# Performance work log

Hardware: AMD Instinct MI355X
Metric: run time of the kernel (lower is better)

## Reference

```python
import jax, jax.numpy as jnp
import numpy as np

DIM = 512
H = 8
HD = DIM // H
MAX_DIST = 128
TABLE = (2 * MAX_DIST + 1) ** 2
LAMBDA_INIT = 0.8


def setup_inputs() -> dict:
    key = jax.random.key(0)
    ks = jax.random.split(key, 20)
    B, Nq, Nkv = 4, 1024, 1024
    inp = {
        "x_q": jax.random.normal(ks[0], (B, Nq, DIM), jnp.float32),
        "x_kv": jax.random.normal(ks[1], (B, Nkv, DIM), jnp.float32),
        "coords_q": jax.random.randint(ks[2], (B, Nq, 2), 0, 256, jnp.int32),
        "coords_k": jax.random.randint(ks[3], (B, Nkv, 2), 0, 256, jnp.int32),
        "alpha_map": jax.random.uniform(ks[4], (B, Nq, 1), jnp.float32),
        "Wq": jax.random.normal(ks[5], (DIM, DIM), jnp.float32) * 0.02,
        "bq": jnp.zeros((DIM,), jnp.float32),
        "Wk": jax.random.normal(ks[6], (DIM, DIM), jnp.float32) * 0.02,
        "bk": jnp.zeros((DIM,), jnp.float32),
        "Wv": jax.random.normal(ks[7], (DIM, DIM), jnp.float32) * 0.02,
        "bv": jnp.zeros((DIM,), jnp.float32),
        "lambda_q1": jax.random.normal(ks[8], (H // 2, HD), jnp.float32) * 0.1,
        "lambda_k1": jax.random.normal(ks[9], (H // 2, HD), jnp.float32) * 0.1,
        "lambda_q2": jax.random.normal(ks[10], (H // 2, HD), jnp.float32) * 0.1,
        "lambda_k2": jax.random.normal(ks[11], (H // 2, HD), jnp.float32) * 0.1,
        "rpe_table": jax.random.normal(ks[12], (TABLE, H), jnp.float32) * 0.02,
        "Wp": jax.random.normal(ks[13], (DIM, DIM), jnp.float32) * 0.02,
        "bp": jnp.zeros((DIM,), jnp.float32),
    }
    return inp


def reference(x_q, x_kv, coords_q, coords_k, alpha_map,
              Wq, bq, Wk, bk, Wv, bv,
              lambda_q1, lambda_k1, lambda_q2, lambda_k2,
              rpe_table, Wp, bp):
    B, Nq, C = x_q.shape
    Nkv = x_kv.shape[1]
    n_half = H // 2
    scale = HD ** -0.5

    # projections -> [B, H, N, HD]
    q = (x_q @ Wq.T + bq).reshape(B, Nq, H, HD).transpose(0, 2, 1, 3)
    k = (x_kv @ Wk.T + bk).reshape(B, Nkv, H, HD).transpose(0, 2, 1, 3)
    v = (x_kv @ Wv.T + bv).reshape(B, Nkv, H, HD).transpose(0, 2, 1, 3)

    # sparse relative position bias: gather per-pair from table
    rel = coords_q[:, :, None, :] - coords_k[:, None, :, :] + MAX_DIST  # [B,Nq,Nkv,2]
    rel = jnp.clip(rel, 0, 2 * MAX_DIST)
    idx = rel[..., 0] * (2 * MAX_DIST + 1) + rel[..., 1]  # [B,Nq,Nkv]
    bias = rpe_table[idx].transpose(0, 3, 1, 2)  # [B,H,Nq,Nkv]

    scores = jnp.einsum('bhqd,bhkd->bhqk', q, k) * scale + bias
    probs = jax.nn.softmax(scores, axis=-1)
    x_std = jnp.einsum('bhqk,bhkd->bhqd', probs, v)

    lam1 = jnp.exp(jnp.sum(lambda_q1 * lambda_k1, axis=-1))  # [n_half]
    lam2 = jnp.exp(jnp.sum(lambda_q2 * lambda_k2, axis=-1))
    lam = (lam1 - lam2 + LAMBDA_INIT)[None, :, None, None]

    attn_diff = probs[:, :n_half] - lam * probs[:, n_half:]
    x_diff = jnp.einsum('bhqk,bhkd->bhqd', attn_diff, v[:, :n_half])

    alpha = alpha_map[:, None]  # [B,1,Nq,1]
    x1 = x_std[:, :n_half] + alpha * x_diff
    x = jnp.concatenate([x1, x_std[:, n_half:]], axis=1)  # [B,H,Nq,HD]
    x = x.transpose(0, 2, 1, 3).reshape(B, Nq, C)
    return x @ Wp.T + bp
```

## Files before the change

### kernel.cpp

```cpp
#include <hip/hip_runtime.h>
#include <cstddef>
#include <cstdint>

#define DIM   512
#define NSEQ  1024
#define NB    4
#define LOG2E 1.44269504f

typedef unsigned short u16;
typedef short bf16x8 __attribute__((ext_vector_type(8)));
typedef _Float16 half8v __attribute__((ext_vector_type(8)));
typedef float f32x4  __attribute__((ext_vector_type(4)));

#define MFMA(a, b, c)  __builtin_amdgcn_mfma_f32_16x16x32_bf16(a, b, c, 0, 0, 0)
#define MFMAH(a, b, c) __builtin_amdgcn_mfma_f32_16x16x32_f16(a, b, c, 0, 0, 0)

__device__ inline void split2(float x, u16& h, u16& l) {
  unsigned u = __float_as_uint(x);
  unsigned hb = (u + 0x7fffu + ((u >> 16) & 1u)) >> 16;
  float fh = __uint_as_float(hb << 16);
  float r = x - fh;
  unsigned v = __float_as_uint(r);
  unsigned lb = (v + 0x7fffu + ((v >> 16) & 1u)) >> 16;
  h = (u16)hb; l = (u16)lb;
}

__device__ inline uint2 pack4(const u16 a[4]) {
  return make_uint2((unsigned)a[0] | ((unsigned)a[1] << 16),
                    (unsigned)a[2] | ((unsigned)a[3] << 16));
}

__device__ inline u16 f2h(float x) {
  _Float16 h = (_Float16)x;
  u16 r; __builtin_memcpy(&r, &h, 2);
  return r;
}
__device__ inline float h2f(u16 b) {
  _Float16 h; __builtin_memcpy(&h, &b, 2);
  return (float)h;
}
__device__ inline unsigned pkh2(float a, float b) {
  return (unsigned)f2h(a) | ((unsigned)f2h(b) << 16);
}

__device__ inline void split_body(const float* __restrict__ in,
                                  u16* __restrict__ out, int e4) {
  const int e = e4 * 4;
  const int m = e >> 9, c = e & 511;
  const float4 v = *(const float4*)(in + e);
  u16 h[4], l[4];
  split2(v.x, h[0], l[0]); split2(v.y, h[1], l[1]);
  split2(v.z, h[2], l[2]); split2(v.w, h[3], l[3]);
  u16* o = out + (size_t)m * 1024 + c;
  *(uint2*)o = pack4(h);
  *(uint2*)(o + 512) = pack4(l);
}

#define GLDS(g, l)                                                        \
  __builtin_amdgcn_global_load_lds(                                       \
      (const __attribute__((address_space(1))) void*)(g),                 \
      (__attribute__((address_space(3))) void*)(l), 16, 0, 0)

__global__ __launch_bounds__(256) void prep(
    const float* __restrict__ wq, const float* __restrict__ wk,
    const float* __restrict__ wv, const float* __restrict__ wp,
    const float* __restrict__ xq, const float* __restrict__ xkv,
    const int* __restrict__ cq, const int* __restrict__ ck,
    const float* __restrict__ rpe,
    u16* __restrict__ w2, u16* __restrict__ xq2, u16* __restrict__ xkv2,
    u16* __restrict__ biasT) {
  __shared__ u16 Ts[8 * 16 * 64];
  const int id = blockIdx.x;
  const int t = threadIdx.x;
  if (id < 1024) {
    const int y = id >> 8;
    const float* src = (y == 0) ? wq : (y == 1) ? wk : (y == 2) ? wv : wp;
    split_body(src, w2 + (size_t)y * 524288, (id & 255) * 256 + t);
  } else if (id < 5120) {
    const int e = id - 1024;
    const int y = e >> 11;
    split_body(y ? xkv : xq, y ? xkv2 : xq2, (e & 2047) * 256 + t);
  } else {
    const int e = id - 5120;
    const int q0 = (e & 15) * 64, k0 = ((e >> 4) & 63) * 16, b = e >> 10;
    const int qn = t & 63, kb = t >> 6;
    const int2 cqv = ((const int2*)cq)[b * NSEQ + q0 + qn];
#pragma unroll
    for (int j = 0; j < 4; ++j) {
      const int k = kb * 4 + j;
      const int2 ckv = ((const int2*)ck)[b * NSEQ + k0 + k];
      const int r0 = min(max(cqv.x - ckv.x + 128, 0), 256);
      const int r1 = min(max(cqv.y - ckv.y + 128, 0), 256);
      const float* rp = rpe + (size_t)(r0 * 257 + r1) * 8;
      const float4 f0 = *(const float4*)rp;
      const float4 f1 = *(const float4*)(rp + 4);
      u16* dst = Ts + k * 64 + qn;
      dst[0 * 1024] = f2h(f0.x * LOG2E); dst[1 * 1024] = f2h(f0.y * LOG2E);
      dst[2 * 1024] = f2h(f0.z * LOG2E); dst[3 * 1024] = f2h(f0.w * LOG2E);
      dst[4 * 1024] = f2h(f1.x * LOG2E); dst[5 * 1024] = f2h(f1.y * LOG2E);
      dst[6 * 1024] = f2h(f1.z * LOG2E); dst[7 * 1024] = f2h(f1.w * LOG2E);
    }
    __syncthreads();
#pragma unroll
    for (int i = 0; i < 4; ++i) {
      const int e2 = i * 256 + t;
      const int row = e2 >> 3, c8 = e2 & 7;
      const int hh = row >> 4, k = row & 15;
      const uint4 v = *(const uint4*)(Ts + row * 64 + c8 * 8);
      *(uint4*)(biasT + ((size_t)(b * 8 + hh) * 1024 + k0 + k) * 1024 +
                q0 + c8 * 8) = v;
    }
  }
}

template <int OUT_MODE>
__device__ __forceinline__ void gemm128(
    u16* __restrict__ Ah, u16* __restrict__ Al,
    u16* __restrict__ Bh, u16* __restrict__ Bl,
    const u16* __restrict__ A2, const u16* __restrict__ B2,
    const float* __restrict__ bias, void* __restrict__ outp,
    float scale, int m0, int n0) {
  const int tid = threadIdx.x;
  const int lane = tid & 63, w = tid >> 6;
  const int wm = (w & 1) * 64, wn = (w >> 1) * 32;
  const int lr = lane >> 3;
  const int scc = (lane & 7) ^ lr;

  const u16* gA = A2 + (size_t)(m0 + w * 32 + lr) * 1024 + scc * 8;
  const u16* gB = B2 + (size_t)(n0 + w * 16 + lr) * 1024 + scc * 8;
  char* lAh = (char*)Ah + w * 4096;  char* lAl = (char*)Al + w * 4096;
  char* lBh = (char*)Bh + w * 2048;  char* lBl = (char*)Bl + w * 2048;

  const int fr = lane & 15, kq = lane >> 4, fx = fr & 7;
  int aoff[2][4], boff[2][2];
#pragma unroll
  for (int s = 0; s < 2; ++s) {
#pragma unroll
    for (int i = 0; i < 4; ++i)
      aoff[s][i] = (wm + i * 16 + fr) * 64 + (((s * 4 + kq) ^ fx)) * 8;
#pragma unroll
    for (int j = 0; j < 2; ++j)
      boff[s][j] = (wn + j * 16 + fr) * 64 + (((s * 4 + kq) ^ fx)) * 8;
  }

  f32x4 acc[4][2] = {};
  for (int k0 = 0; k0 < 512; k0 += 64) {
    __syncthreads();
#pragma unroll
    for (int i = 0; i < 4; ++i) {
      GLDS(gA + (size_t)i * 8192 + k0, lAh + i * 1024);
      GLDS(gA + (size_t)i * 8192 + 512 + k0, lAl + i * 1024);
    }
#pragma unroll
    for (int i = 0; i < 2; ++i) {
      GLDS(gB + (size_t)i * 8192 + k0, lBh + i * 1024);
      GLDS(gB + (size_t)i * 8192 + 512 + k0, lBl + i * 1024);
    }
    __syncthreads();
#pragma unroll
    for (int s = 0; s < 2; ++s) {
      bf16x8 ah[4], al[4], bh[2], bl[2];
#pragma unroll
      for (int i = 0; i < 4; ++i) {
        ah[i] = *(const bf16x8*)(Ah + aoff[s][i]);
        al[i] = *(const bf16x8*)(Al + aoff[s][i]);
      }
#pragma unroll
      for (int j = 0; j < 2; ++j) {
        bh[j] = *(const bf16x8*)(Bh + boff[s][j]);
        bl[j] = *(const bf16x8*)(Bl + boff[s][j]);
      }
#pragma unroll
      for (int i = 0; i < 4; ++i)
#pragma unroll
        for (int j = 0; j < 2; ++j) {
          acc[i][j] = MFMA(al[i], bh[j], acc[i][j]);
          acc[i][j] = MFMA(ah[i], bl[j], acc[i][j]);
          acc[i][j] = MFMA(ah[i], bh[j], acc[i][j]);
        }
    }
  }

  const int er = (lane >> 4) * 4, ec = lane & 15;
#pragma unroll
  for (int i = 0; i < 4; ++i)
#pragma unroll
    for (int j = 0; j < 2; ++j) {
      const int row = m0 + wm + i * 16 + er;
      const int col = n0 + wn + j * 16 + ec;
      const float bv = bias[col];
      if (OUT_MODE == 4) {
        u16 hf[4];
#pragma unroll
        for (int r = 0; r < 4; ++r) hf[r] = f2h((acc[i][j][r] + bv) * scale);
        const int bb = row >> 10, kk = row & 1023;
        *(uint2*)((u16*)outp + ((size_t)(bb * 512 + col)) * 1024 + kk) =
            pack4(hf);
      } else {
#pragma unroll
        for (int r = 0; r < 4; ++r) {
          const float v = (acc[i][j][r] + bv) * scale;
          if (OUT_MODE == 3)
            ((u16*)outp)[(size_t)(row + r) * 512 + col] = f2h(v);
          else
            ((float*)outp)[(size_t)(row + r) * 512 + col] = v;
        }
      }
    }
}

__global__ __launch_bounds__(256, 3) void gemm_qkv(
    const u16* __restrict__ xq2, const u16* __restrict__ xkv2,
    const u16* __restrict__ w2, const float* __restrict__ bq,
    const float* __restrict__ bk, const float* __restrict__ bv,
    u16* __restrict__ q2f, u16* __restrict__ k2f, u16* __restrict__ vtf) {
  __shared__ __align__(16) u16 Ah[8192], Al[8192], Bh[4096], Bl[4096];
  const int z = blockIdx.z;
  const int m0 = blockIdx.x * 128, n0 = blockIdx.y * 64;
  if (z == 0)
    gemm128<3>(Ah, Al, Bh, Bl, xq2, w2, bq, q2f, 0.125f * LOG2E, m0, n0);
  else if (z == 1)
    gemm128<3>(Ah, Al, Bh, Bl, xkv2, w2 + 524288, bk, k2f, 1.0f, m0, n0);
  else
    gemm128<4>(Ah, Al, Bh, Bl, xkv2, w2 + 2 * 524288, bv, vtf, 1.0f, m0, n0);
}

__global__ __launch_bounds__(256, 3) void gemm_out(
    const u16* __restrict__ xa2, const u16* __restrict__ w2p,
    const float* __restrict__ bp, float* __restrict__ out) {
  __shared__ __align__(16) u16 Ah[8192], Al[8192], Bh[4096], Bl[4096];
  gemm128<0>(Ah, Al, Bh, Bl, xa2, w2p, bp, out, 1.0f,
             blockIdx.x * 128, blockIdx.y * 64);
}

__global__ __launch_bounds__(512) void attn_f16(
    const u16* __restrict__ q2f, const u16* __restrict__ k2f,
    const u16* __restrict__ vtf, const float* __restrict__ amap,
    const float* __restrict__ lq1, const float* __restrict__ lk1,
    const float* __restrict__ lq2, const float* __restrict__ lk2,
    const u16* __restrict__ biasT, u16* __restrict__ xo) {
  __shared__ __align__(16) u16 KsL[2][2][4096];
  __shared__ __align__(16) u16 VtL[2][2][4096];
  __shared__ float2 mls[2][2][2][16];
  __shared__ float l2s[32];
  __shared__ float lam_s;

  const int tid = threadIdx.x;
  const int lane = tid & 63, w = tid >> 6;
  const int kg = w >> 2, h = (w >> 1) & 1, qs = w & 1;
  const int wl = w & 3;
  const int hp = blockIdx.y, b = blockIdx.z;
  const int q0 = blockIdx.x * 32;
  const int head = hp + 4 * h;
  const int lq = lane & 15, lg = lane >> 4;
  const int q = qs * 16 + lq;
  const size_t qrow = (size_t)(b * NSEQ + q0 + q);

  if (tid < 64) {
    float p1 = lq1[hp * 64 + tid] * lk1[hp * 64 + tid];
    float p2 = lq2[hp * 64 + tid] * lk2[hp * 64 + tid];
#pragma unroll
    for (int m = 32; m >= 1; m >>= 1) {
      p1 += __shfl_xor(p1, m, 64);
      p2 += __shfl_xor(p2, m, 64);
    }
    if (tid == 0) lam_s = __expf(p1) - __expf(p2) + 0.8f;
  }

  const float alpha = amap[qrow];

  half8v Qf[2];
#pragma unroll
  for (int ks = 0; ks < 2; ++ks)
    Qf[ks] = *(const half8v*)(q2f + qrow * 512 + head * 64 + ks * 32 + lg * 8);

  f32x4 Ya[4] = {};
  f32x4 Yb[4] = {};
  float m_run = -1e30f, l_run = 0.0f;

  const int lr = lane >> 3;
  const int lc = (lane & 7) ^ lr;
  const int cw = wl * 2;

  auto stage = [&](int it, int p) {
    const int kbase = kg * 512 + it * 32;
#pragma unroll
    for (int i = 0; i < 2; ++i) {
      const int c = cw + i;
      const int row = c * 8 + lr;
      const int sh = row >> 5, k = row & 31;
      const u16* src = k2f + (size_t)(b * NSEQ + kbase + k) * 512 +
                       (hp + 4 * sh) * 64 + lc * 8;
      GLDS(src, (char*)KsL[kg][p] + c * 1024);
    }
#pragma unroll
    for (int i = 0; i < 2; ++i) {
      const int c = cw + i;
      const int d = c * 8 + lr;
      const int hv = lc >> 2, kc = lc & 3;
      const u16* src = vtf + (size_t)(b * 512 + (hp + 4 * hv) * 64 + d) * 1024 +
                       kbase + kc * 8;
      GLDS(src, (char*)VtL[kg][p] + c * 1024);
    }
  };

  const u16* bT = biasT + ((size_t)(b * 8 + head) << 20) + q0 + q;

  stage(0, 0);

  for (int it = 0; it < 16; ++it) {
    const int p = it & 1;
    __syncthreads();
    if (it + 1 < 16) stage(it + 1, p ^ 1);

    u16 rb[8];
    {
      const u16* bt = bT + (size_t)(kg * 512 + it * 32) * 1024;
#pragma unroll
      for (int kt = 0; kt < 2; ++kt)
#pragma unroll
        for (int r = 0; r < 4; ++r)
          rb[kt * 4 + r] = bt[(size_t)(kt * 16 + lg * 4 + r) * 1024];
    }

    const u16* Kb = KsL[kg][p];
    f32x4 st[2] = {};
#pragma unroll
    for (int kt = 0; kt < 2; ++kt) {
      const int krow = kt * 16 + lq;
      const int rx = krow & 7;
#pragma unroll
      for (int ks = 0; ks < 2; ++ks) {
        const int phys = (ks * 4 + lg) ^ rx;
        const half8v kf = *(const half8v*)(Kb + (h * 32 + krow) * 64 + phys * 8);
        st[kt] = MFMAH(kf, Qf[ks], st[kt]);
      }
    }

    float sv[2][4];
    float mx = -1e30f;
#pragma unroll
    for (int kt = 0; kt < 2; ++kt)
#pragma unroll
      for (int r = 0; r < 4; ++r) {
        const float s = st[kt][r] + h2f(rb[kt * 4 + r]);
        sv[kt][r] = s;
        mx = fmaxf(mx, s);
      }
    mx = fmaxf(mx, __shfl_xor(mx, 16, 64));
    mx = fmaxf(mx, __shfl_xor(mx, 32, 64));
    const float mnew = fmaxf(m_run, mx);
    const float a = exp2f(m_run - mnew);
    m_run = mnew;
    float pr[2][4], ps = 0.0f;
#pragma unroll
    for (int kt = 0; kt < 2; ++kt)
#pragma unroll
      for (int r = 0; r < 4; ++r) {
        pr[kt][r] = exp2f(sv[kt][r] - mnew);
        ps += pr[kt][r];
      }
    ps += __shfl_xor(ps, 16, 64);
    ps += __shfl_xor(ps, 32, 64);
    l_run = l_run * a + ps;
#pragma unroll
    for (int dt = 0; dt < 4; ++dt) Ya[dt] *= a;
    if (h == 1) {
#pragma unroll
      for (int dt = 0; dt < 4; ++dt) Yb[dt] *= a;
    }

    const unsigned a0 = pkh2(pr[0][0], pr[0][1]);
    const unsigned a1 = pkh2(pr[0][2], pr[0][3]);
    const unsigned b0 = pkh2(pr[1][0], pr[1][1]);
    const unsigned b1 = pkh2(pr[1][2], pr[1][3]);
    const int srcA = lq + ((lg & 1) << 5);
    const unsigned A0 = __shfl((int)a0, srcA),      A1 = __shfl((int)a1, srcA);
    const unsigned B0 = __shfl((int)b0, srcA),      B1 = __shfl((int)b1, srcA);
    const unsigned C0 = __shfl((int)a0, srcA + 16), C1 = __shfl((int)a1, srcA + 16);
    const unsigned D0 = __shfl((int)b0, srcA + 16), D1 = __shfl((int)b1, srcA + 16);
    const bool t2 = lg >= 2;
    const uint4 Pu = make_uint4(t2 ? B0 : A0, t2 ? B1 : A1,
                                t2 ? D0 : C0, t2 ? D1 : C1);
    half8v pb;
    __builtin_memcpy(&pb, &Pu, 16);

    const u16* Vb = VtL[kg][p];
    if (h == 0) {
#pragma unroll
      for (int dt = 0; dt < 4; ++dt) {
        const int d = dt * 16 + lq;
        const half8v v1 = *(const half8v*)(Vb + d * 64 + ((lg ^ (d & 7))) * 8);
        Ya[dt] = MFMAH(v1, pb, Ya[dt]);
      }
    } else {
#pragma unroll
      for (int dt = 0; dt < 4; ++dt) {
        const int d = dt * 16 + lq;
        const int dx = d & 7;
        const half8v v1 = *(const half8v*)(Vb + d * 64 + ((lg ^ dx)) * 8);
        Yb[dt] = MFMAH(v1, pb, Yb[dt]);
        const half8v v2 = *(const half8v*)(Vb + d * 64 + (((4 + lg) ^ dx)) * 8);
        Ya[dt] = MFMAH(v2, pb, Ya[dt]);
      }
    }
  }

  float* mY = (float*)KsL;
  float* mB = (float*)VtL;
  __syncthreads();
  if (lane < 16) mls[kg][h][qs][lane] = make_float2(m_run, l_run);
  if (kg == 1) {
#pragma unroll
    for (int dt = 0; dt < 4; ++dt)
#pragma unroll
      for (int r = 0; r < 4; ++r)
        mY[((h * 2 + qs) * 64 + lane) * 16 + dt * 4 + r] = Ya[dt][r];
    if (h == 1) {
#pragma unroll
      for (int dt = 0; dt < 4; ++dt)
#pragma unroll
        for (int r = 0; r < 4; ++r)
          mB[(qs * 64 + lane) * 16 + dt * 4 + r] = Yb[dt][r];
    }
  }
  __syncthreads();
  float l_tot = l_run;
  if (kg == 0) {
    const float2 o = mls[1][h][qs][lq];
    const float mm = fmaxf(m_run, o.x);
    const float s0 = exp2f(m_run - mm);
    const float s1 = exp2f(o.x - mm);
    l_tot = l_run * s0 + o.y * s1;
    const float* sY = mY + ((h * 2 + qs) * 64 + lane) * 16;
#pragma unroll
    for (int dt = 0; dt < 4; ++dt)
#pragma unroll
      for (int r = 0; r < 4; ++r)
        Ya[dt][r] = Ya[dt][r] * s0 + sY[dt * 4 + r] * s1;
    if (h == 1) {
      const float* sB = mB + (qs * 64 + lane) * 16;
#pragma unroll
      for (int dt = 0; dt < 4; ++dt)
#pragma unroll
        for (int r = 0; r < 4; ++r)
          Yb[dt][r] = Yb[dt][r] * s0 + sB[dt * 4 + r] * s1;
    }
  }

  __syncthreads();
  float* y2x = (float*)KsL;
  if (kg == 0 && h == 1) {
    if (lane < 16) l2s[qs * 16 + lane] = l_tot;
#pragma unroll
    for (int dt = 0; dt < 4; ++dt)
#pragma unroll
      for (int r = 0; r < 4; ++r)
        y2x[(qs * 64 + lane) * 16 + dt * 4 + r] = Yb[dt][r];
  }
  __syncthreads();
  if (kg == 0 && h == 1) {
    const float inv2 = 1.0f / l_tot;
#pragma unroll
    for (int dt = 0; dt < 4; ++dt) {
      u16 hh[4], ll[4];
#pragma unroll
      for (int r = 0; r < 4; ++r) split2(Ya[dt][r] * inv2, hh[r], ll[r]);
      u16* o = xo + qrow * 1024 + (hp + 4) * 64 + dt * 16 + lg * 4;
      *(uint2*)o = pack4(hh);
      *(uint2*)(o + 512) = pack4(ll);
    }
  } else if (kg == 0 && h == 0) {
    const float inv1 = 1.0f / l_tot;
    const float inv2 = 1.0f / l2s[qs * 16 + lq];
    const float c1 = (1.0f + alpha) * inv1;
    const float c2 = alpha * lam_s * inv2;
#pragma unroll
    for (int dt = 0; dt < 4; ++dt) {
      u16 hh[4], ll[4];
#pragma unroll
      for (int r = 0; r < 4; ++r) {
        const float y2 = y2x[(qs * 64 + lane) * 16 + dt * 4 + r];
        split2(c1 * Ya[dt][r] - c2 * y2, hh[r], ll[r]);
      }
      u16* o = xo + qrow * 1024 + hp * 64 + dt * 16 + lg * 4;
      *(uint2*)o = pack4(hh);
      *(uint2*)(o + 512) = pack4(ll);
    }
  }
}

extern "C" void kernel_launch(void* const* d_in, const int* in_sizes, int n_in,
                              void* d_out, int out_size, void* d_ws, size_t ws_size,
                              hipStream_t stream) {
  const float* x_q   = (const float*)d_in[0];
  const float* x_kv  = (const float*)d_in[1];
  const int*   c_q   = (const int*)d_in[2];
  const int*   c_k   = (const int*)d_in[3];
  const float* alpha = (const float*)d_in[4];
  const float* Wq    = (const float*)d_in[5];
  const float* bq    = (const float*)d_in[6];
  const float* Wk    = (const float*)d_in[7];
  const float* bk    = (const float*)d_in[8];
  const float* Wv    = (const float*)d_in[9];
  const float* bv    = (const float*)d_in[10];
  const float* lq1   = (const float*)d_in[11];
  const float* lk1   = (const float*)d_in[12];
  const float* lq2   = (const float*)d_in[13];
  const float* lk2   = (const float*)d_in[14];
  const float* rpe   = (const float*)d_in[15];
  const float* Wp    = (const float*)d_in[16];
  const float* bp    = (const float*)d_in[17];

  u16* w2    = (u16*)d_ws;
  u16* xq2   = (u16*)((char*)d_ws + (4u << 20));
  u16* q2f   = (u16*)((char*)d_ws + (12u << 20));
  u16* k2f   = (u16*)((char*)d_ws + (16u << 20));
  u16* vtf   = (u16*)((char*)d_ws + (20u << 20));
  u16* xa    = xq2;
  u16* biasT = (u16*)((char*)d_ws + (28u << 20));
  u16* xkv2  = (u16*)d_out;

  prep<<<9216, 256, 0, stream>>>(Wq, Wk, Wv, Wp, x_q, x_kv, c_q, c_k, rpe,
                                 w2, xq2, xkv2, biasT);
  gemm_qkv<<<dim3(32, 8, 3), 256, 0, stream>>>(xq2, xkv2, w2, bq, bk, bv,
                                               q2f, k2f, vtf);
  attn_f16<<<dim3(32, 4, NB), 512, 0, stream>>>(
      q2f, k2f, vtf, alpha, lq1, lk1, lq2, lk2, biasT, xa);
  gemm_out<<<dim3(32, 8), 256, 0, stream>>>(xa, w2 + 3 * 524288, bp,
                                            (float*)d_out);
}
```

Before: 207.0 us.

## Double-buffer LDS in split-bf16 GEMMs and widen tiles to 128x128

Replaces the single-buffered GEMM with a double-buffered version. The next K-slice (32 wide, hi and lo halves packed into one buffer) is loaded into LDS while MFMAs run on the current slice, leaving one barrier per iteration instead of two. The output tile grows from 128x64 to 128x128, so each wave computes 4x4 fragments. This halves the grid for the QKV and output projections and cuts the occupancy hint from 3 to 2 blocks per CU. It trades more registers and shared memory per block and fewer blocks for better latency hiding and operand reuse.

```diff
diff --git a/kernel.cpp b/kernel.cpp
--- a/kernel.cpp
+++ b/kernel.cpp
@@ -114,78 +114,74 @@
 }
 
 template <int OUT_MODE>
-__device__ __forceinline__ void gemm128(
-    u16* __restrict__ Ah, u16* __restrict__ Al,
-    u16* __restrict__ Bh, u16* __restrict__ Bl,
+__device__ __forceinline__ void gemm_db(
+    u16 (*__restrict__ As)[8192], u16 (*__restrict__ Bs)[8192],
     const u16* __restrict__ A2, const u16* __restrict__ B2,
     const float* __restrict__ bias, void* __restrict__ outp,
     float scale, int m0, int n0) {
   const int tid = threadIdx.x;
   const int lane = tid & 63, w = tid >> 6;
-  const int wm = (w & 1) * 64, wn = (w >> 1) * 32;
-  const int lr = lane >> 3;
-  const int scc = (lane & 7) ^ lr;
-
-  const u16* gA = A2 + (size_t)(m0 + w * 32 + lr) * 1024 + scc * 8;
-  const u16* gB = B2 + (size_t)(n0 + w * 16 + lr) * 1024 + scc * 8;
-  char* lAh = (char*)Ah + w * 4096;  char* lAl = (char*)Al + w * 4096;
-  char* lBh = (char*)Bh + w * 2048;  char* lBl = (char*)Bl + w * 2048;
+  const int wm = (w & 1) * 64, wn = (w >> 1) * 64;
+  const int lr8 = lane >> 3;
+  const int scc = (lane & 7) ^ lr8;
+  const int colA = ((scc & 3) * 8) + ((scc >> 2) * 512);
 
   const int fr = lane & 15, kq = lane >> 4, fx = fr & 7;
-  int aoff[2][4], boff[2][2];
-#pragma unroll
-  for (int s = 0; s < 2; ++s) {
+  int aoh[4], aol[4], boh[4], bol[4];
+#pragma unroll
+  for (int i = 0; i < 4; ++i) {
+    const int ra = (wm + i * 16 + fr) * 64;
+    aoh[i] = ra + ((kq ^ fx)) * 8;
+    aol[i] = ra + (((4 + kq) ^ fx)) * 8;
+    const int rb = (wn + i * 16 + fr) * 64;
+    boh[i] = rb + ((kq ^ fx)) * 8;
+    bol[i] = rb + (((4 + kq) ^ fx)) * 8;
+  }
+
+  auto stage = [&](int it, int p) {
+    const int k0 = it * 32;
+#pragma unroll
+    for (int i = 0; i < 4; ++i) {
+      const int rA = m0 + w * 32 + i * 8 + lr8;
+      GLDS(A2 + (size_t)rA * 1024 + colA + k0,
+           (char*)As[p] + (w * 32 + i * 8) * 128);
+      const int rB = n0 + w * 32 + i * 8 + lr8;
+      GLDS(B2 + (size_t)rB * 1024 + colA + k0,
+           (char*)Bs[p] + (w * 32 + i * 8) * 128);
+    }
+  };
+
+  f32x4 acc[4][4] = {};
+  stage(0, 0);
+  for (int it = 0; it < 16; ++it) {
+    const int p = it & 1;
+    __syncthreads();
+    if (it + 1 < 16) stage(it + 1, p ^ 1);
+    const u16* Ab = As[p];
+    const u16* Bb = Bs[p];
+    bf16x8 ah[4], al[4], bh[4], bl[4];
+#pragma unroll
+    for (int i = 0; i < 4; ++i) {
+      ah[i] = *(const bf16x8*)(Ab + aoh[i]);
+      al[i] = *(const bf16x8*)(Ab + aol[i]);
+      bh[i] = *(const bf16x8*)(Bb + boh[i]);
+      bl[i] = *(const bf16x8*)(Bb + bol[i]);
+    }
 #pragma unroll
     for (int i = 0; i < 4; ++i)
-      aoff[s][i] = (wm + i * 16 + fr) * 64 + (((s * 4 + kq) ^ fx)) * 8;
-#pragma unroll
-    for (int j = 0; j < 2; ++j)
-      boff[s][j] = (wn + j * 16 + fr) * 64 + (((s * 4 + kq) ^ fx)) * 8;
-  }
-
-  f32x4 acc[4][2] = {};
-  for (int k0 = 0; k0 < 512; k0 += 64) {
-    __syncthreads();
-#pragma unroll
-    for (int i = 0; i < 4; ++i) {
-      GLDS(gA + (size_t)i * 8192 + k0, lAh + i * 1024);
-      GLDS(gA + (size_t)i * 8192 + 512 + k0, lAl + i * 1024);
-    }
-#pragma unroll
-    for (int i = 0; i < 2; ++i) {
-      GLDS(gB + (size_t)i * 8192 + k0, lBh + i * 1024);
-      GLDS(gB + (size_t)i * 8192 + 512 + k0, lBl + i * 1024);
-    }
-    __syncthreads();
-#pragma unroll
-    for (int s = 0; s < 2; ++s) {
-      bf16x8 ah[4], al[4], bh[2], bl[2];
-#pragma unroll
-      for (int i = 0; i < 4; ++i) {
-        ah[i] = *(const bf16x8*)(Ah + aoff[s][i]);
-        al[i] = *(const bf16x8*)(Al + aoff[s][i]);
-      }
-#pragma unroll
-      for (int j = 0; j < 2; ++j) {
-        bh[j] = *(const bf16x8*)(Bh + boff[s][j]);
-        bl[j] = *(const bf16x8*)(Bl + boff[s][j]);
-      }
-#pragma unroll
-      for (int i = 0; i < 4; ++i)
-#pragma unroll
-        for (int j = 0; j < 2; ++j) {
-          acc[i][j] = MFMA(al[i], bh[j], acc[i][j]);
-          acc[i][j] = MFMA(ah[i], bl[j], acc[i][j]);
-          acc[i][j] = MFMA(ah[i], bh[j], acc[i][j]);
-        }
-    }
+#pragma unroll
+      for (int j = 0; j < 4; ++j) {
+        acc[i][j] = MFMA(al[i], bh[j], acc[i][j]);
+        acc[i][j] = MFMA(ah[i], bl[j], acc[i][j]);
+        acc[i][j] = MFMA(ah[i], bh[j], acc[i][j]);
+      }
   }
 
   const int er = (lane >> 4) * 4, ec = lane & 15;
 #pragma unroll
   for (int i = 0; i < 4; ++i)
 #pragma unroll
-    for (int j = 0; j < 2; ++j) {
+    for (int j = 0; j < 4; ++j) {
       const int row = m0 + wm + i * 16 + er;
       const int col = n0 + wn + j * 16 + ec;
       const float bv = bias[col];
@@ -209,28 +205,28 @@
     }
 }
 
-__global__ __launch_bounds__(256, 3) void gemm_qkv(
+__global__ __launch_bounds__(256, 2) void gemm_qkv(
     const u16* __restrict__ xq2, const u16* __restrict__ xkv2,
     const u16* __restrict__ w2, const float* __restrict__ bq,
     const float* __restrict__ bk, const float* __restrict__ bv,
     u16* __restrict__ q2f, u16* __restrict__ k2f, u16* __restrict__ vtf) {
-  __shared__ __align__(16) u16 Ah[8192], Al[8192], Bh[4096], Bl[4096];
+  __shared__ __align__(16) u16 As[2][8192], Bs[2][8192];
   const int z = blockIdx.z;
-  const int m0 = blockIdx.x * 128, n0 = blockIdx.y * 64;
+  const int m0 = blockIdx.x * 128, n0 = blockIdx.y * 128;
   if (z == 0)
-    gemm128<3>(Ah, Al, Bh, Bl, xq2, w2, bq, q2f, 0.125f * LOG2E, m0, n0);
+    gemm_db<3>(As, Bs, xq2, w2, bq, q2f, 0.125f * LOG2E, m0, n0);
   else if (z == 1)
-    gemm128<3>(Ah, Al, Bh, Bl, xkv2, w2 + 524288, bk, k2f, 1.0f, m0, n0);
+    gemm_db<3>(As, Bs, xkv2, w2 + 524288, bk, k2f, 1.0f, m0, n0);
   else
-    gemm128<4>(Ah, Al, Bh, Bl, xkv2, w2 + 2 * 524288, bv, vtf, 1.0f, m0, n0);
-}
-
-__global__ __launch_bounds__(256, 3) void gemm_out(
+    gemm_db<4>(As, Bs, xkv2, w2 + 2 * 524288, bv, vtf, 1.0f, m0, n0);
+}
+
+__global__ __launch_bounds__(256, 2) void gemm_out(
     const u16* __restrict__ xa2, const u16* __restrict__ w2p,
     const float* __restrict__ bp, float* __restrict__ out) {
-  __shared__ __align__(16) u16 Ah[8192], Al[8192], Bh[4096], Bl[4096];
-  gemm128<0>(Ah, Al, Bh, Bl, xa2, w2p, bp, out, 1.0f,
-             blockIdx.x * 128, blockIdx.y * 64);
+  __shared__ __align__(16) u16 As[2][8192], Bs[2][8192];
+  gemm_db<0>(As, Bs, xa2, w2p, bp, out, 1.0f,
+             blockIdx.x * 128, blockIdx.y * 128);
 }
 
 __global__ __launch_bounds__(512) void attn_f16(
@@ -523,10 +519,10 @@
 
   prep<<<9216, 256, 0, stream>>>(Wq, Wk, Wv, Wp, x_q, x_kv, c_q, c_k, rpe,
                                  w2, xq2, xkv2, biasT);
-  gemm_qkv<<<dim3(32, 8, 3), 256, 0, stream>>>(xq2, xkv2, w2, bq, bk, bv,
+  gemm_qkv<<<dim3(32, 4, 3), 256, 0, stream>>>(xq2, xkv2, w2, bq, bk, bv,
                                                q2f, k2f, vtf);
   attn_f16<<<dim3(32, 4, NB), 512, 0, stream>>>(
       q2f, k2f, vtf, alpha, lq1, lk1, lq2, lk2, biasT, xa);
-  gemm_out<<<dim3(32, 8), 256, 0, stream>>>(xa, w2 + 3 * 524288, bp,
+  gemm_out<<<dim3(32, 4), 256, 0, stream>>>(xa, w2 + 3 * 524288, bp,
                                             (float*)d_out);
 }
```

New measurement: 210.4 us. About the same (+1.6%).
